# Kernel tuning notes

Measured on AMD Instinct MI355X. Metric: run time of the kernel, lower is better.

Reference implementation:

```python
import jax, jax.numpy as jnp
import numpy as np

GS = 256      # grid/node count
PARAM = 128   # feature width
KC = 32       # keepconst (constant features)
I1, I2 = 64, 32
PK = PARAM - KC
K_DIV = 16.0  # neighbor-count normalizer
EPS = 1e-3    # Keras BatchNorm default epsilon
B = 4


def _bn(x, g, b, m, v):
    # inference-mode batch norm over last axis
    return (x - m) * jax.lax.rsqrt(v + EPS) * g + b


def setup_inputs() -> dict:
    key = jax.random.key(0)
    ks = jax.random.split(key, 24)
    mat = (jax.random.uniform(ks[0], (B, GS, GS)) < (K_DIV / GS)).astype(jnp.float32)
    val = jax.random.normal(ks[1], (B, GS, PARAM), dtype=jnp.float32)
    def w(k, shape):
        fan = shape[0] if len(shape) > 1 else shape[0]
        return jax.random.normal(k, shape, dtype=jnp.float32) * (1.0 / np.sqrt(fan))
    inp = {
        'mat': mat, 'val': val,
        'M1': w(ks[2], (2 * PARAM, I1)), 'B1': 0.05 * jax.random.normal(ks[3], (I1,)),
        'M2': w(ks[4], (I1, I2)),        'B2': 0.05 * jax.random.normal(ks[5], (I2,)),
        'M3': w(ks[6], (I2, PK)),        'B3': 0.05 * jax.random.normal(ks[7], (PK,)),
    }
    for idx, d in zip((1, 2, 3), (I1, I2, PK)):
        kk = jax.random.split(ks[7 + idx], 4)
        inp[f'g{idx}'] = 1.0 + 0.1 * jax.random.normal(kk[0], (d,), dtype=jnp.float32)
        inp[f'b{idx}'] = 0.1 * jax.random.normal(kk[1], (d,), dtype=jnp.float32)
        inp[f'm{idx}'] = 0.1 * jax.random.normal(kk[2], (d,), dtype=jnp.float32)
        inp[f'v{idx}'] = jax.random.uniform(kk[3], (d,), dtype=jnp.float32, minval=0.5, maxval=1.5)
    return inp


def reference(mat, val, M1, B1, M2, B2, M3, B3,
              g1, b1, m1, v1, g2, b2, m2, v2, g3, b3, m3, v3):
    con = val[:, :, :KC]
    # selector matmuls == gather: pair i -> (a=i//GS, b=i%GS)
    feat = jnp.repeat(val, GS, axis=1)          # (B, GS*GS, PARAM) = val_a
    vb = jnp.tile(val, (1, GS, 1))              # (B, GS*GS, PARAM) = val_b
    premlp = jnp.concatenate([feat, vb - feat], axis=-1)  # (B, GS*GS, 2*PARAM)
    s = jax.nn.relu(_bn(premlp @ M1 + B1, g1, b1, m1, v1))
    s = jax.nn.relu(_bn(s @ M2 + B2, g2, b2, m2, v2))
    s = jax.nn.relu(_bn(s @ M3 + B3, g3, b3, m3, v3))      # (B, GS*GS, PK)
    res = s.reshape(val.shape[0], GS, GS, PK)               # (B, a, b, PK)
    # masked scatter-sum over neighbor axis b
    summ = jnp.einsum('babk,bab->bak'.replace('a', 'x').replace('b', 'y', 1), res, mat) if False else \
        jnp.einsum('bxyk,bxy->bxk', res, mat)               # (B, GS, PK)
    var = jnp.clip(summ / K_DIV, -1.0, 1.0)                 # advrelu([-1,1]) == clip
    return jnp.concatenate([con, var], axis=-1)             # (B, GS, PARAM)
```

## Files before the change

kernel.cpp:

```cpp
#include <hip/hip_runtime.h>

#define GS    256
#define PARAM 128
#define KC    32
#define I1    64
#define I2    32
#define PK    96
#define B_    4
#define NROWS (B_ * GS)
#define EPS   1e-3f
#define KDIV_INV (1.0f / 16.0f)
#define CHUNK 32

constexpr int U_OFF   = 0;
constexpr int W_OFF   = NROWS * I1;
constexpr int M2F_OFF = 2 * NROWS * I1;
constexpr int C2_OFF  = M2F_OFF + I1 * I2;
constexpr int M3F_OFF = C2_OFF + I2;
constexpr int C3_OFF  = M3F_OFF + I2 * PK;
constexpr int C1_OFF  = C3_OFF + PK;

__global__ __launch_bounds__(256) void glmlp_precompute(
    const float* __restrict__ val, const float* __restrict__ M1,
    const float* __restrict__ B1,
    const float* __restrict__ M2, const float* __restrict__ B2,
    const float* __restrict__ M3, const float* __restrict__ B3,
    const float* __restrict__ g1, const float* __restrict__ b1,
    const float* __restrict__ m1, const float* __restrict__ v1,
    const float* __restrict__ g2, const float* __restrict__ b2,
    const float* __restrict__ m2, const float* __restrict__ v2,
    const float* __restrict__ g3, const float* __restrict__ b3,
    const float* __restrict__ m3, const float* __restrict__ v3,
    float* __restrict__ ws, float* __restrict__ out)
{
    const int blk = blockIdx.x;
    const int t = threadIdx.x;

    if (blk < NROWS) {
        __shared__ float vrow[PARAM];
        __shared__ float red[4][I1];
        const int r = blk;
        if (t < PARAM) vrow[t] = val[r * PARAM + t];
        __syncthreads();

        if (t < KC) out[r * PARAM + t] = vrow[t];

        const int i = t & (I1 - 1);
        const int q = t >> 6;
        const float* __restrict__ Mb = M1 + ((q >> 1) ? (PARAM * I1) : 0);
        const int p0 = (q & 1) * 64;
        float acc = 0.f;
        #pragma unroll 8
        for (int p = 0; p < 64; ++p)
            acc = fmaf(vrow[p0 + p], Mb[(p0 + p) * I1 + i], acc);
        red[q][i] = acc;
        __syncthreads();

        if (q == 0) {
            const float T  = red[0][i] + red[1][i];
            const float Wv = red[2][i] + red[3][i];
            const float s1 = g1[i] * rsqrtf(v1[i] + EPS);
            ws[U_OFF + r * I1 + i] = (T - Wv) * s1;
            ws[W_OFF + r * I1 + i] = Wv * s1;
        }
    } else {
        if (t < I1) {
            const float s1 = g1[t] * rsqrtf(v1[t] + EPS);
            ws[C1_OFF + t] = B1[t] * s1 + b1[t] - m1[t] * s1;
        }
        if (t < I2) {
            const float s2 = g2[t] * rsqrtf(v2[t] + EPS);
            ws[C2_OFF + t] = B2[t] * s2 + b2[t] - m2[t] * s2;
        }
        if (t < PK) {
            const float s3 = g3[t] * rsqrtf(v3[t] + EPS);
            ws[C3_OFF + t] = B3[t] * s3 + b3[t] - m3[t] * s3;
        }
        for (int idx = t; idx < I1 * I2; idx += 256) {
            const int j = idx & (I2 - 1);
            const float s2 = g2[j] * rsqrtf(v2[j] + EPS);
            ws[M2F_OFF + idx] = M2[idx] * s2;
        }
        for (int idx = t; idx < I2 * PK; idx += 256) {
            const int k = idx % PK;
            const float s3 = g3[k] * rsqrtf(v3[k] + EPS);
            ws[M3F_OFF + idx] = M3[idx] * s3;
        }
    }
}

__global__ __launch_bounds__(256) void glmlp_pairs(
    const float* __restrict__ mat, const float* __restrict__ ws,
    float* __restrict__ out)
{
    __shared__ float m2s[I1 * I2];
    __shared__ float uxs[I1];
    __shared__ float c2s[I2];
    __shared__ float c3s[PK];
    __shared__ float H1[CHUNK][I1];
    __shared__ float H2[CHUNK][I2];
    __shared__ int   acty[GS];
    __shared__ float partial[2][PK];
    __shared__ int   cnt;

    const int r = blockIdx.x;
    const int t = threadIdx.x;
    const int wbase = (r & ~(GS - 1));
    const float* __restrict__ W = ws + W_OFF;

    if (t == 0) cnt = 0;
    for (int idx = t; idx < I1 * I2; idx += 256) m2s[idx] = ws[M2F_OFF + idx];
    if (t < I2) c2s[t] = ws[C2_OFF + t];
    if (t < PK) c3s[t] = ws[C3_OFF + t];
    if (t < I1) uxs[t] = ws[U_OFF + r * I1 + t] + ws[C1_OFF + t];
    const float mv = mat[r * GS + t];

    const bool l3 = (t < 2 * PK);
    const int k = l3 ? (t % PK) : 0;
    const int h = l3 ? (t / PK) : 0;
    float m3col[I2];
    if (l3) {
        #pragma unroll
        for (int ii = 0; ii < I2; ++ii) m3col[ii] = ws[M3F_OFF + ii * PK + k];
    }
    __syncthreads();

    if (mv != 0.0f) acty[atomicAdd(&cnt, 1)] = t;
    __syncthreads();
    const int n = cnt;

    float acc = 0.0f;

    for (int base = 0; base < n; base += CHUNK) {
        const int nc = min(CHUNK, n - base);

        for (int idx = t; idx < nc * I1; idx += 256) {
            const int p = idx >> 6, i = idx & (I1 - 1);
            const int y = acty[base + p];
            H1[p][i] = fmaxf(uxs[i] + W[(wbase + y) * I1 + i], 0.0f);
        }
        __syncthreads();

        for (int idx = t; idx < nc * I2; idx += 256) {
            const int p = idx >> 5, j = idx & (I2 - 1);
            float a = c2s[j];
            const float4* h1p4 = (const float4*)(&H1[p][0]);
            #pragma unroll
            for (int i4 = 0; i4 < I1 / 4; ++i4) {
                const float4 hv = h1p4[i4];
                const int i = i4 * 4;
                a = fmaf(hv.x, m2s[(i + 0) * I2 + j], a);
                a = fmaf(hv.y, m2s[(i + 1) * I2 + j], a);
                a = fmaf(hv.z, m2s[(i + 2) * I2 + j], a);
                a = fmaf(hv.w, m2s[(i + 3) * I2 + j], a);
            }
            H2[p][j] = fmaxf(a, 0.0f);
        }
        __syncthreads();

        if (l3) {
            int p = h;
            for (; p + 2 < nc; p += 4) {
                float a0 = c3s[k], a1 = c3s[k];
                const float4* A4 = (const float4*)(&H2[p][0]);
                const float4* B4 = (const float4*)(&H2[p + 2][0]);
                #pragma unroll
                for (int i4 = 0; i4 < I2 / 4; ++i4) {
                    const float4 ha = A4[i4];
                    const float4 hb = B4[i4];
                    const int i = i4 * 4;
                    a0 = fmaf(ha.x, m3col[i + 0], a0);
                    a1 = fmaf(hb.x, m3col[i + 0], a1);
                    a0 = fmaf(ha.y, m3col[i + 1], a0);
                    a1 = fmaf(hb.y, m3col[i + 1], a1);
                    a0 = fmaf(ha.z, m3col[i + 2], a0);
                    a1 = fmaf(hb.z, m3col[i + 2], a1);
                    a0 = fmaf(ha.w, m3col[i + 3], a0);
                    a1 = fmaf(hb.w, m3col[i + 3], a1);
                }
                acc += fmaxf(a0, 0.0f) + fmaxf(a1, 0.0f);
            }
            for (; p < nc; p += 2) {
                float a0 = c3s[k];
                const float4* A4 = (const float4*)(&H2[p][0]);
                #pragma unroll
                for (int i4 = 0; i4 < I2 / 4; ++i4) {
                    const float4 ha = A4[i4];
                    const int i = i4 * 4;
                    a0 = fmaf(ha.x, m3col[i + 0], a0);
                    a0 = fmaf(ha.y, m3col[i + 1], a0);
                    a0 = fmaf(ha.z, m3col[i + 2], a0);
                    a0 = fmaf(ha.w, m3col[i + 3], a0);
                }
                acc += fmaxf(a0, 0.0f);
            }
        }
    }

    if (l3) partial[h][k] = acc;
    __syncthreads();

    if (t < PK) {
        float v = (partial[0][t] + partial[1][t]) * KDIV_INV;
        v = fminf(fmaxf(v, -1.0f), 1.0f);
        out[r * PARAM + KC + t] = v;
    }
}

extern "C" void kernel_launch(void* const* d_in, const int* in_sizes, int n_in,
                              void* d_out, int out_size, void* d_ws, size_t ws_size,
                              hipStream_t stream) {
    const float* mat = (const float*)d_in[0];
    const float* val = (const float*)d_in[1];
    const float* M1  = (const float*)d_in[2];
    const float* B1  = (const float*)d_in[3];
    const float* M2  = (const float*)d_in[4];
    const float* B2  = (const float*)d_in[5];
    const float* M3  = (const float*)d_in[6];
    const float* B3  = (const float*)d_in[7];
    const float* g1  = (const float*)d_in[8];
    const float* b1  = (const float*)d_in[9];
    const float* m1  = (const float*)d_in[10];
    const float* v1  = (const float*)d_in[11];
    const float* g2  = (const float*)d_in[12];
    const float* b2  = (const float*)d_in[13];
    const float* m2  = (const float*)d_in[14];
    const float* v2  = (const float*)d_in[15];
    const float* g3  = (const float*)d_in[16];
    const float* b3  = (const float*)d_in[17];
    const float* m3  = (const float*)d_in[18];
    const float* v3  = (const float*)d_in[19];

    float* ws  = (float*)d_ws;
    float* out = (float*)d_out;

    hipLaunchKernelGGL(glmlp_precompute, dim3(NROWS + 1), dim3(256), 0, stream,
                       val, M1, B1, M2, B2, M3, B3,
                       g1, b1, m1, v1, g2, b2, m2, v2, g3, b3, m3, v3,
                       ws, out);

    hipLaunchKernelGGL(glmlp_pairs, dim3(NROWS), dim3(256), 0, stream,
                       mat, ws, out);
}
```

Before: 124.4 us.

## Fuse precompute into pair kernel, recomputing neighbor layer-1 projection per block

Merges the precompute and pair kernels into one launch, folding batch-norm constants per block and dropping the workspace. The neighbor half of the first layer (val_y · M1b) is now recomputed per block from gathered neighbor rows instead of read from a precomputed table. This removes a launch and the workspace round trip. In exchange, the layer-1 arithmetic for neighbors is duplicated across rows, and M1b is streamed from global memory in every block.

```diff
diff --git a/kernel.cpp b/kernel.cpp
--- a/kernel.cpp
+++ b/kernel.cpp
@@ -11,18 +11,11 @@
 #define EPS   1e-3f
 #define KDIV_INV (1.0f / 16.0f)
 #define CHUNK 32
-
-constexpr int U_OFF   = 0;
-constexpr int W_OFF   = NROWS * I1;
-constexpr int M2F_OFF = 2 * NROWS * I1;
-constexpr int C2_OFF  = M2F_OFF + I1 * I2;
-constexpr int M3F_OFF = C2_OFF + I2;
-constexpr int C3_OFF  = M3F_OFF + I2 * PK;
-constexpr int C1_OFF  = C3_OFF + PK;
-
-__global__ __launch_bounds__(256) void glmlp_precompute(
-    const float* __restrict__ val, const float* __restrict__ M1,
-    const float* __restrict__ B1,
+#define VYP   132
+
+__global__ __launch_bounds__(256, 4) void glmlp_fused(
+    const float* __restrict__ mat, const float* __restrict__ val,
+    const float* __restrict__ M1, const float* __restrict__ B1,
     const float* __restrict__ M2, const float* __restrict__ B2,
     const float* __restrict__ M3, const float* __restrict__ B3,
     const float* __restrict__ g1, const float* __restrict__ b1,
@@ -31,20 +24,57 @@
     const float* __restrict__ m2, const float* __restrict__ v2,
     const float* __restrict__ g3, const float* __restrict__ b3,
     const float* __restrict__ m3, const float* __restrict__ v3,
-    float* __restrict__ ws, float* __restrict__ out)
+    float* __restrict__ out)
 {
-    const int blk = blockIdx.x;
+    __shared__ float vrow[PARAM];
+    __shared__ float uxs[I1];
+    __shared__ float s1s[I1];
+    __shared__ float m2s[I1 * I2];
+    __shared__ float c2s[I2];
+    __shared__ float vy[CHUNK][VYP];
+    __shared__ float H1[CHUNK][I1];
+    __shared__ float H2[CHUNK][I2];
+    __shared__ int   acty[GS];
+    __shared__ float partial[2][PK];
+    __shared__ int   cnt;
+
+    float (&red)[4][I1] = *reinterpret_cast<float (*)[4][I1]>(&H1[0][0]);
+
+    const int r = blockIdx.x;
     const int t = threadIdx.x;
-
-    if (blk < NROWS) {
-        __shared__ float vrow[PARAM];
-        __shared__ float red[4][I1];
-        const int r = blk;
-        if (t < PARAM) vrow[t] = val[r * PARAM + t];
-        __syncthreads();
-
-        if (t < KC) out[r * PARAM + t] = vrow[t];
-
+    const int wbase = r & ~(GS - 1);
+
+    if (t == 0) cnt = 0;
+    if (t < PARAM) vrow[t] = val[r * PARAM + t];
+    const float mv = mat[r * GS + t];
+
+    const bool l3 = (t < 2 * PK);
+    const int k = t % PK;
+    const int h = t / PK;
+    float m3col[I2];
+    float c3k = 0.0f;
+    if (l3) {
+        const float s3 = g3[k] * rsqrtf(v3[k] + EPS);
+        c3k = (B3[k] - m3[k]) * s3 + b3[k];
+        #pragma unroll
+        for (int ii = 0; ii < I2; ++ii) m3col[ii] = M3[ii * PK + k] * s3;
+    }
+
+    for (int idx = t; idx < I1 * I2; idx += 256) {
+        const int j = idx & (I2 - 1);
+        m2s[idx] = M2[idx] * g2[j] * rsqrtf(v2[j] + EPS);
+    }
+    if (t < I2) {
+        const float s2 = g2[t] * rsqrtf(v2[t] + EPS);
+        c2s[t] = (B2[t] - m2[t]) * s2 + b2[t];
+    }
+    __syncthreads();
+
+    if (mv != 0.0f) acty[atomicAdd(&cnt, 1)] = t;
+
+    if (t < KC) out[r * PARAM + t] = vrow[t];
+
+    {
         const int i = t & (I1 - 1);
         const int q = t >> 6;
         const float* __restrict__ Mb = M1 + ((q >> 1) ? (PARAM * I1) : 0);
@@ -54,97 +84,65 @@
         for (int p = 0; p < 64; ++p)
             acc = fmaf(vrow[p0 + p], Mb[(p0 + p) * I1 + i], acc);
         red[q][i] = acc;
-        __syncthreads();
-
-        if (q == 0) {
-            const float T  = red[0][i] + red[1][i];
-            const float Wv = red[2][i] + red[3][i];
-            const float s1 = g1[i] * rsqrtf(v1[i] + EPS);
-            ws[U_OFF + r * I1 + i] = (T - Wv) * s1;
-            ws[W_OFF + r * I1 + i] = Wv * s1;
-        }
-    } else {
-        if (t < I1) {
-            const float s1 = g1[t] * rsqrtf(v1[t] + EPS);
-            ws[C1_OFF + t] = B1[t] * s1 + b1[t] - m1[t] * s1;
-        }
-        if (t < I2) {
-            const float s2 = g2[t] * rsqrtf(v2[t] + EPS);
-            ws[C2_OFF + t] = B2[t] * s2 + b2[t] - m2[t] * s2;
-        }
-        if (t < PK) {
-            const float s3 = g3[t] * rsqrtf(v3[t] + EPS);
-            ws[C3_OFF + t] = B3[t] * s3 + b3[t] - m3[t] * s3;
-        }
-        for (int idx = t; idx < I1 * I2; idx += 256) {
-            const int j = idx & (I2 - 1);
-            const float s2 = g2[j] * rsqrtf(v2[j] + EPS);
-            ws[M2F_OFF + idx] = M2[idx] * s2;
-        }
-        for (int idx = t; idx < I2 * PK; idx += 256) {
-            const int k = idx % PK;
-            const float s3 = g3[k] * rsqrtf(v3[k] + EPS);
-            ws[M3F_OFF + idx] = M3[idx] * s3;
-        }
-    }
-}
-
-__global__ __launch_bounds__(256) void glmlp_pairs(
-    const float* __restrict__ mat, const float* __restrict__ ws,
-    float* __restrict__ out)
-{
-    __shared__ float m2s[I1 * I2];
-    __shared__ float uxs[I1];
-    __shared__ float c2s[I2];
-    __shared__ float c3s[PK];
-    __shared__ float H1[CHUNK][I1];
-    __shared__ float H2[CHUNK][I2];
-    __shared__ int   acty[GS];
-    __shared__ float partial[2][PK];
-    __shared__ int   cnt;
-
-    const int r = blockIdx.x;
-    const int t = threadIdx.x;
-    const int wbase = (r & ~(GS - 1));
-    const float* __restrict__ W = ws + W_OFF;
-
-    if (t == 0) cnt = 0;
-    for (int idx = t; idx < I1 * I2; idx += 256) m2s[idx] = ws[M2F_OFF + idx];
-    if (t < I2) c2s[t] = ws[C2_OFF + t];
-    if (t < PK) c3s[t] = ws[C3_OFF + t];
-    if (t < I1) uxs[t] = ws[U_OFF + r * I1 + t] + ws[C1_OFF + t];
-    const float mv = mat[r * GS + t];
-
-    const bool l3 = (t < 2 * PK);
-    const int k = l3 ? (t % PK) : 0;
-    const int h = l3 ? (t / PK) : 0;
-    float m3col[I2];
-    if (l3) {
-        #pragma unroll
-        for (int ii = 0; ii < I2; ++ii) m3col[ii] = ws[M3F_OFF + ii * PK + k];
-    }
-    __syncthreads();
-
-    if (mv != 0.0f) acty[atomicAdd(&cnt, 1)] = t;
+    }
     __syncthreads();
     const int n = cnt;
 
-    float acc = 0.0f;
+    if (t < I1) {
+        const float s1 = g1[t] * rsqrtf(v1[t] + EPS);
+        const float c1 = (B1[t] - m1[t]) * s1 + b1[t];
+        s1s[t] = s1;
+        uxs[t] = (red[0][t] + red[1][t] - red[2][t] - red[3][t]) * s1 + c1;
+    }
+    __syncthreads();
+
+    const float* __restrict__ M1b = M1 + PARAM * I1;
+    float accO = 0.0f;
 
     for (int base = 0; base < n; base += CHUNK) {
         const int nc = min(CHUNK, n - base);
 
-        for (int idx = t; idx < nc * I1; idx += 256) {
-            const int p = idx >> 6, i = idx & (I1 - 1);
-            const int y = acty[base + p];
-            H1[p][i] = fmaxf(uxs[i] + W[(wbase + y) * I1 + i], 0.0f);
+        for (int idx = t; idx < nc * (PARAM / 4); idx += 256) {
+            const int yy = idx >> 5;
+            const int pq = idx & 31;
+            const float4 v4 =
+                ((const float4*)&val[(wbase + acty[base + yy]) * PARAM])[pq];
+            *(float4*)&vy[yy][pq * 4] = v4;
+        }
+        __syncthreads();
+
+        {
+            const int i = t & (I1 - 1);
+            const int g = t >> 6;
+            const float s1 = s1s[i];
+            const float ux = uxs[i];
+            float acc[8] = {0.f, 0.f, 0.f, 0.f, 0.f, 0.f, 0.f, 0.f};
+            for (int p = 0; p < PARAM; p += 4) {
+                const float w0 = M1b[(p + 0) * I1 + i];
+                const float w1 = M1b[(p + 1) * I1 + i];
+                const float w2 = M1b[(p + 2) * I1 + i];
+                const float w3 = M1b[(p + 3) * I1 + i];
+                #pragma unroll
+                for (int j = 0; j < 8; ++j) {
+                    const float4 vv = *(const float4*)&vy[g + 4 * j][p];
+                    acc[j] = fmaf(vv.x, w0, acc[j]);
+                    acc[j] = fmaf(vv.y, w1, acc[j]);
+                    acc[j] = fmaf(vv.z, w2, acc[j]);
+                    acc[j] = fmaf(vv.w, w3, acc[j]);
+                }
+            }
+            #pragma unroll
+            for (int j = 0; j < 8; ++j) {
+                const int yy = g + 4 * j;
+                if (yy < nc) H1[yy][i] = fmaxf(ux + acc[j] * s1, 0.f);
+            }
         }
         __syncthreads();
 
         for (int idx = t; idx < nc * I2; idx += 256) {
             const int p = idx >> 5, j = idx & (I2 - 1);
             float a = c2s[j];
-            const float4* h1p4 = (const float4*)(&H1[p][0]);
+            const float4* h1p4 = (const float4*)&H1[p][0];
             #pragma unroll
             for (int i4 = 0; i4 < I1 / 4; ++i4) {
                 const float4 hv = h1p4[i4];
@@ -154,16 +152,16 @@
                 a = fmaf(hv.z, m2s[(i + 2) * I2 + j], a);
                 a = fmaf(hv.w, m2s[(i + 3) * I2 + j], a);
             }
-            H2[p][j] = fmaxf(a, 0.0f);
+            H2[p][j] = fmaxf(a, 0.f);
         }
         __syncthreads();
 
         if (l3) {
             int p = h;
             for (; p + 2 < nc; p += 4) {
-                float a0 = c3s[k], a1 = c3s[k];
-                const float4* A4 = (const float4*)(&H2[p][0]);
-                const float4* B4 = (const float4*)(&H2[p + 2][0]);
+                float a0 = c3k, a1 = c3k;
+                const float4* A4 = (const float4*)&H2[p][0];
+                const float4* B4 = (const float4*)&H2[p + 2][0];
                 #pragma unroll
                 for (int i4 = 0; i4 < I2 / 4; ++i4) {
                     const float4 ha = A4[i4];
@@ -178,11 +176,11 @@
                     a0 = fmaf(ha.w, m3col[i + 3], a0);
                     a1 = fmaf(hb.w, m3col[i + 3], a1);
                 }
-                acc += fmaxf(a0, 0.0f) + fmaxf(a1, 0.0f);
+                accO += fmaxf(a0, 0.f) + fmaxf(a1, 0.f);
             }
             for (; p < nc; p += 2) {
-                float a0 = c3s[k];
-                const float4* A4 = (const float4*)(&H2[p][0]);
+                float a0 = c3k;
+                const float4* A4 = (const float4*)&H2[p][0];
                 #pragma unroll
                 for (int i4 = 0; i4 < I2 / 4; ++i4) {
                     const float4 ha = A4[i4];
@@ -192,12 +190,12 @@
                     a0 = fmaf(ha.z, m3col[i + 2], a0);
                     a0 = fmaf(ha.w, m3col[i + 3], a0);
                 }
-                acc += fmaxf(a0, 0.0f);
-            }
-        }
-    }
-
-    if (l3) partial[h][k] = acc;
+                accO += fmaxf(a0, 0.f);
+            }
+        }
+    }
+
+    if (l3) partial[h][k] = accO;
     __syncthreads();
 
     if (t < PK) {
@@ -231,14 +229,10 @@
     const float* m3  = (const float*)d_in[18];
     const float* v3  = (const float*)d_in[19];
 
-    float* ws  = (float*)d_ws;
     float* out = (float*)d_out;
 
-    hipLaunchKernelGGL(glmlp_precompute, dim3(NROWS + 1), dim3(256), 0, stream,
-                       val, M1, B1, M2, B2, M3, B3,
+    hipLaunchKernelGGL(glmlp_fused, dim3(NROWS), dim3(256), 0, stream,
+                       mat, val, M1, B1, M2, B2, M3, B3,
                        g1, b1, m1, v1, g2, b2, m2, v2, g3, b3, m3, v3,
-                       ws, out);
-
-    hipLaunchKernelGGL(glmlp_pairs, dim3(NROWS), dim3(256), 0, stream,
-                       mat, ws, out);
+                       out);
 }
```

Result: slower. 182.7 us (+46.8%).
